# Performance work log

Hardware: AMD Instinct MI355X
Metric: run time of the kernel (lower is better)

The kernel has to match this reference:

```python
import jax, jax.numpy as jnp
import numpy as np

RHO = 0.5
MASK = 1.0
FR0 = 4096  # ifft length along fast-time axis
FR1 = 512   # fft length along slow-time (Doppler) axis
WIN = 8     # sliding-window length of the phase-reference accumulator
EPS_DENOM = 1e-6


def setup_inputs() -> dict:
    key = jax.random.key(0)
    k1, k2 = jax.random.split(key)
    x_real = jax.random.normal(k1, (8, 4096, 256), dtype=jnp.float32)
    x_imag = jax.random.normal(k2, (8, 4096, 256), dtype=jnp.float32)
    return {"x_real": x_real, "x_imag": x_imag}


def _phase_com_doppler(inp):
    # inp: [B, N, M_in] complex; ifft along last axis padded/truncated to FR0
    final = jnp.fft.ifft(inp, n=FR0, axis=2)  # [B, N, M]
    B, N, M = final.shape
    out0 = final[:, 0, :]                      # [B, M]
    # reproduces the torch `if k < 7` branch without control flow.
    buf0 = jnp.zeros((WIN, B, M), final.dtype).at[WIN - 1].set(out0)

    def step(carry, f_k1):
        pref, buf = carry
        s = jnp.sum(jnp.conj(pref) * f_k1, axis=-1, keepdims=True)  # [B,1]
        phase = s / jnp.abs(s)
        o = f_k1 * jnp.conj(phase)                                  # [B,M]
        pref = pref + o - buf[0]
        buf = jnp.concatenate([buf[1:], o[None]], axis=0)
        return (pref, buf), o

    seq = jnp.swapaxes(final, 0, 1)[1:]        # [N-1, B, M]
    _, outs = jax.lax.scan(step, (out0, buf0), seq)
    out = jnp.concatenate([out0[None], outs], axis=0)  # [N, B, M]
    out = jnp.swapaxes(out, 0, 1)              # [B, N, M]
    # fft along pulse axis padded to FR1
    return jnp.fft.fft(out, n=FR1, axis=1)     # [B, FR1, M]


def reference(x_real, x_imag):
    x = jax.lax.complex(x_real, x_imag)        # [B, P, Q] complex64
    denom = MASK + RHO
    denom = EPS_DENOM if denom == 0 else denom
    x2 = x * (1.0 / denom)
    out3 = _phase_com_doppler(jnp.swapaxes(x2, -1, -2))  # [B, FR1, FR0]
    out3 = jnp.swapaxes(out3, -1, -2)          # [B, FR0, FR1]
    # cs_data dict -> tuple ('input', 'nnline_input')
    return (x, out3)
```

## Files before the change

kernel.cpp:

```cpp
#include <hip/hip_runtime.h>
#include <math.h>

#define NF 4096
#define NC 256
#define NJ 512
#define CH 128
#define TWO_PI_F 6.28318530717958647692f

__device__ __forceinline__ float2 cmul(float2 a, float2 b) {
    return make_float2(a.x*b.x - a.y*b.y, a.x*b.y + a.y*b.x);
}

__device__ __forceinline__ void dft4i(float2& x0, float2& x1, float2& x2, float2& x3, float sgn) {
    float2 t0 = make_float2(x0.x + x2.x, x0.y + x2.y);
    float2 t1 = make_float2(x0.x - x2.x, x0.y - x2.y);
    float2 t2 = make_float2(x1.x + x3.x, x1.y + x3.y);
    float2 t3 = make_float2(x1.x - x3.x, x1.y - x3.y);
    float2 it3 = make_float2(-sgn * t3.y, sgn * t3.x);
    x0 = make_float2(t0.x + t2.x, t0.y + t2.y);
    x2 = make_float2(t0.x - t2.x, t0.y - t2.y);
    x1 = make_float2(t1.x + it3.x, t1.y + it3.y);
    x3 = make_float2(t1.x - it3.x, t1.y - it3.y);
}

__device__ __forceinline__ void dft16(float2* u, float sgn) {
    dft4i(u[0], u[4], u[8],  u[12], sgn);
    dft4i(u[1], u[5], u[9],  u[13], sgn);
    dft4i(u[2], u[6], u[10], u[14], sgn);
    dft4i(u[3], u[7], u[11], u[15], sgn);
    const float C1 = 0.9238795325112867f, S1 = 0.3826834323650898f, R2 = 0.7071067811865476f;
    u[5]  = cmul(u[5],  make_float2(C1,  sgn * S1));
    u[6]  = cmul(u[6],  make_float2(R2,  sgn * R2));
    u[7]  = cmul(u[7],  make_float2(S1,  sgn * C1));
    u[9]  = cmul(u[9],  make_float2(R2,  sgn * R2));
    u[10] = cmul(u[10], make_float2(0.f, sgn));
    u[11] = cmul(u[11], make_float2(-R2, sgn * R2));
    u[13] = cmul(u[13], make_float2(S1,  sgn * C1));
    u[14] = cmul(u[14], make_float2(-R2, sgn * R2));
    u[15] = cmul(u[15], make_float2(-C1, -sgn * S1));
    dft4i(u[0],  u[1],  u[2],  u[3],  sgn);
    dft4i(u[4],  u[5],  u[6],  u[7],  sgn);
    dft4i(u[8],  u[9],  u[10], u[11], sgn);
    dft4i(u[12], u[13], u[14], u[15], sgn);
}

__device__ __forceinline__ void dft8(const float2* u, float2* v, float sgn) {
    float2 e0 = u[0], e1 = u[2], e2 = u[4], e3 = u[6];
    float2 o0 = u[1], o1 = u[3], o2 = u[5], o3 = u[7];
    dft4i(e0, e1, e2, e3, sgn);
    dft4i(o0, o1, o2, o3, sgn);
    const float R2 = 0.7071067811865476f;
    float2 w1 = make_float2(R2, sgn * R2);
    float2 w2 = make_float2(0.f, sgn);
    float2 w3 = make_float2(-R2, sgn * R2);
    float2 t1 = cmul(o1, w1), t2 = cmul(o2, w2), t3 = cmul(o3, w3);
    v[0] = make_float2(e0.x + o0.x, e0.y + o0.y);
    v[4] = make_float2(e0.x - o0.x, e0.y - o0.y);
    v[1] = make_float2(e1.x + t1.x, e1.y + t1.y);
    v[5] = make_float2(e1.x - t1.x, e1.y - t1.y);
    v[2] = make_float2(e2.x + t2.x, e2.y + t2.y);
    v[6] = make_float2(e2.x - t2.x, e2.y - t2.y);
    v[3] = make_float2(e3.x + t3.x, e3.y + t3.y);
    v[7] = make_float2(e3.x - t3.x, e3.y - t3.y);
}

__global__ __launch_bounds__(256) void transpose_kernel(const float* __restrict__ xr,
                                                        const float* __restrict__ xi,
                                                        float2* __restrict__ fin,
                                                        int b0, int nbm1, int nbshift) {
    __shared__ float ldr[64][65];
    __shared__ float ldi[64][65];
    int wg = blockIdx.x;
    int bl = wg & nbm1;
    int rest = wg >> nbshift;
    int ft = rest & 63;
    int ct = rest >> 6;
    int f0 = ft << 6, c0 = ct << 6;
    int t = threadIdx.x;
    int cl = t & 63;
    int rq = t >> 6;
    const float scale = 1.0f / (4096.0f * 1.5f);
    int bg = b0 + bl;
    const float* xrb = xr + (size_t)bg * NF * NC;
    const float* xib = xi + (size_t)bg * NF * NC;
#pragma unroll
    for (int q = 0; q < 16; q++) {
        int r = q * 4 + rq;
        size_t idx = (size_t)(f0 + r) * NC + c0 + cl;
        ldr[cl][r] = xrb[idx] * scale;
        ldi[cl][r] = xib[idx] * scale;
    }
    __syncthreads();
    int fl = t & 63;
#pragma unroll
    for (int q = 0; q < 16; q++) {
        int cr = q * 4 + rq;
        fin[((size_t)(bl * NC + c0 + cr)) * NF + f0 + fl] =
            make_float2(ldr[cr][fl], ldi[cr][fl]);
    }
}

#define IPAD(a) ((a) + ((a) >> 4))

template<int P>
__device__ __forceinline__ void pass16(float2* S, int t, float sgn) {
    const int k = t & (P - 1);
    float2 u[16];
#pragma unroll
    for (int r = 0; r < 16; r++) u[r] = S[IPAD(t + 256 * r)];
    __syncthreads();
    if (P > 1) {
        float ab = sgn * (TWO_PI_F / (16.0f * (float)P)) * (float)k;
#pragma unroll
        for (int r = 1; r < 16; r++) {
            float sn, cs; __sincosf(ab * (float)r, &sn, &cs);
            u[r] = cmul(u[r], make_float2(cs, sn));
        }
    }
    dft16(u, sgn);
    const int base = 16 * P * (t / P) + k;
#pragma unroll
    for (int j = 0; j < 16; j++) {
        const int sl = ((j & 3) << 2) | (j >> 2);
        S[IPAD(base + j * P)] = u[sl];
    }
    __syncthreads();
}

__global__ __launch_bounds__(256) void ifft4096_kernel(float2* __restrict__ fin,
                                                       int bmask, int bshift) {
    __shared__ float2 S[4352];
    int wg = blockIdx.x;
    int bl = wg & bmask;
    int c = wg >> bshift;
    int t = threadIdx.x;
    size_t base = ((size_t)(bl * NC + c)) * NF;
#pragma unroll
    for (int q = 0; q < 16; q++) {
        int f = t + 256 * q;
        S[IPAD(f)] = fin[base + f];
    }
    __syncthreads();
    pass16<1>(S, t, 1.0f);
    pass16<16>(S, t, 1.0f);
    pass16<256>(S, t, 1.0f);
#pragma unroll
    for (int q = 0; q < 16; q++) {
        int f = t + 256 * q;
        fin[base + f] = S[IPAD(f)];
    }
}

__global__ __launch_bounds__(256) void gram_kernel(const float2* __restrict__ fin,
                                                   float2* __restrict__ gpart) {
    __shared__ float2 ring[16][CH];
    int wg = blockIdx.x;
    int bl = wg >> 7;
    int ch = (wg >> 2) & 31;
    int ks = wg & 3;
    int m0 = ch * CH;
    int k0 = ks * 64;
    int kend = k0 + 64;
    int t = threadIdx.x;
    int dgrp = t >> 5;
    int lane = t & 31;
    for (int r = (k0 >= 8 ? k0 - 8 : 0); r <= k0; r++)
        if (t < CH) ring[r & 15][t] = fin[((size_t)(bl * NC + r)) * NF + m0 + t];
    __syncthreads();
    for (int k = k0; k < kend; k++) {
        float2 nxt;
        bool ld = (k + 1 < kend) && (t < CH);
        if (ld) nxt = fin[((size_t)(bl * NC + k + 1)) * NF + m0 + t];
        int d = dgrp + 1;
        float2 acc = make_float2(0.f, 0.f);
        if (k - d >= 0) {
            int sk = k & 15, sj = (k - d) & 15;
#pragma unroll
            for (int i = 0; i < 4; i++) {
                int m = lane + 32 * i;
                float2 a = ring[sj][m];
                float2 bb = ring[sk][m];
                acc.x += a.x * bb.x + a.y * bb.y;
                acc.y += a.x * bb.y - a.y * bb.x;
            }
        }
#pragma unroll
        for (int off = 16; off >= 1; off >>= 1) {
            acc.x += __shfl_xor(acc.x, off);
            acc.y += __shfl_xor(acc.y, off);
        }
        if (lane == 0)
            gpart[((size_t)(bl * 32 + ch) * NC + k) * 8 + dgrp] = acc;
        if (ld) ring[(k + 1) & 15][t] = nxt;
        __syncthreads();
    }
}

__global__ void gsum_kernel(const float2* __restrict__ gpart, float2* __restrict__ gs, int total) {
    int e = blockIdx.x * blockDim.x + threadIdx.x;
    if (e >= total) return;
    int bl = e >> 11;
    int kd = e & 2047;
    float2 s = make_float2(0.f, 0.f);
    for (int ch = 0; ch < 32; ch++) {
        float2 v = gpart[((size_t)(bl * 32 + ch)) * 2048 + kd];
        s.x += v.x; s.y += v.y;
    }
    gs[e] = s;
}

#define SCAN_STEP(A0, A1, A2, A3, KIDX)  do {                                  \
    float rx0 = p1.x*A0.x - p1.y*A0.y, ry0 = p1.x*A0.y + p1.y*A0.x;            \
    float rx1 = p2.x*A0.z - p2.y*A0.w, ry1 = p2.x*A0.w + p2.y*A0.z;            \
    float rx2 = p3.x*A1.x - p3.y*A1.y, ry2 = p3.x*A1.y + p3.y*A1.x;            \
    float rx3 = p4.x*A1.z - p4.y*A1.w, ry3 = p4.x*A1.w + p4.y*A1.z;            \
    float rx4 = p5.x*A2.x - p5.y*A2.y, ry4 = p5.x*A2.y + p5.y*A2.x;            \
    float rx5 = p6.x*A2.z - p6.y*A2.w, ry5 = p6.x*A2.w + p6.y*A2.z;            \
    float rx6 = p7.x*A3.x - p7.y*A3.y, ry6 = p7.x*A3.y + p7.y*A3.x;            \
    float rx7 = p8.x*A3.z - p8.y*A3.w, ry7 = p8.x*A3.w + p8.y*A3.z;            \
    float sx = ((rx0 + rx1) + (rx2 + rx3)) + ((rx4 + rx5) + (rx6 + rx7));      \
    float sy = ((ry0 + ry1) + (ry2 + ry3)) + ((ry4 + ry5) + (ry6 + ry7));      \
    float inv = rsqrtf(sx * sx + sy * sy);                                     \
    float2 np = make_float2(sx * inv, sy * inv);                               \
    phase[t * NC + (KIDX)] = np;                                               \
    p8 = p7; p7 = p6; p6 = p5; p5 = p4; p4 = p3; p3 = p2; p2 = p1; p1 = np;    \
} while (0)

#define SCAN_LOADG4(BUF, KBASE)  do {                                          \
    _Pragma("unroll") for (int j = 0; j < 4; j++) {                            \
        _Pragma("unroll") for (int q = 0; q < 4; q++)                          \
            BUF[j][q] = gb4[((KBASE) + j) * 4 + q];                            \
    }                                                                          \
} while (0)

#define SCAN_GRP4(BUF, KBASE, FIRST)  do {                                     \
    _Pragma("unroll") for (int j = 0; j < 4; j++) {                            \
        if (FIRST && j == 0) {                                                 \
            phase[t * NC] = make_float2(1.f, 0.f);                             \
        } else {                                                               \
            SCAN_STEP(BUF[j][0], BUF[j][1], BUF[j][2], BUF[j][3], (KBASE) + j);\
        }                                                                      \
    }                                                                          \
} while (0)

__global__ __launch_bounds__(64, 1) void scan_copy_kernel(const float2* __restrict__ gs,
                                                          float2* __restrict__ phase, int nb,
                                                          const float4* __restrict__ csrc,
                                                          float4* __restrict__ cdst, int cn4) {
    if (blockIdx.x != 0) {
        int i = (blockIdx.x - 1) * 64 + threadIdx.x;
        int stride = (gridDim.x - 1) * 64;
        for (; i < cn4; i += stride) cdst[i] = csrc[i];
        return;
    }
    int t = threadIdx.x;
    if (t >= nb) return;
    const float4* gb4 = (const float4*)(gs + (size_t)t * 2048);
    float2 z = make_float2(0.f, 0.f);
    float2 p1 = make_float2(1.f, 0.f);
    float2 p2 = z, p3 = z, p4 = z, p5 = z, p6 = z, p7 = z, p8 = z;
    float4 GA[4][4], GB[4][4];
    SCAN_LOADG4(GA, 0);
    for (int g2 = 0; g2 < 32; g2++) {
        int k0 = g2 * 8;
        SCAN_LOADG4(GB, k0 + 4);
        __builtin_amdgcn_sched_barrier(0);
        if (g2 == 0) { SCAN_GRP4(GA, k0, true); } else { SCAN_GRP4(GA, k0, false); }
        if (g2 < 31) SCAN_LOADG4(GA, k0 + 8);
        __builtin_amdgcn_sched_barrier(0);
        SCAN_GRP4(GB, k0 + 4, false);
    }
}

__global__ void scale_kernel(float4* __restrict__ fin4, const float2* __restrict__ phase, int n4) {
    int i = blockIdx.x * blockDim.x + threadIdx.x;
    if (i >= n4) return;
    int row = i >> 11;
    float2 ph = phase[row];
    float4 v = fin4[i];
    fin4[i] = make_float4(v.x*ph.x + v.y*ph.y, v.y*ph.x - v.x*ph.y,
                          v.z*ph.x + v.w*ph.y, v.w*ph.x - v.z*ph.y);
}

#define FPAD 516

template<int P, bool ZTOP>
__device__ __forceinline__ void pass8x(float2* L, int fp, int i2, float sgn) {
    const int ia = i2, ib = i2 + 32;
    const int ka = ia & (P - 1), kb = ib & (P - 1);
    float2 ua[8], ub[8];
#pragma unroll
    for (int r = 0; r < 8; r++) {
        if (ZTOP && r >= 4) {
            ua[r] = make_float2(0.f, 0.f);
            ub[r] = make_float2(0.f, 0.f);
        } else {
            ua[r] = L[fp * FPAD + ia + 64 * r];
            ub[r] = L[fp * FPAD + ib + 64 * r];
        }
    }
    __syncthreads();
    if (P > 1) {
        float aba = sgn * (TWO_PI_F / (8.0f * (float)P)) * (float)ka;
        float abb = sgn * (TWO_PI_F / (8.0f * (float)P)) * (float)kb;
#pragma unroll
        for (int r = 1; r < 8; r++) {
            float sn, cs;
            __sincosf(aba * (float)r, &sn, &cs);
            ua[r] = cmul(ua[r], make_float2(cs, sn));
            __sincosf(abb * (float)r, &sn, &cs);
            ub[r] = cmul(ub[r], make_float2(cs, sn));
        }
    }
    float2 va[8], vb[8];
    dft8(ua, va, sgn);
    dft8(ub, vb, sgn);
    const int basea = 8 * P * (ia / P) + ka;
    const int baseb = 8 * P * (ib / P) + kb;
#pragma unroll
    for (int r = 0; r < 8; r++) {
        L[fp * FPAD + basea + r * P] = va[r];
        L[fp * FPAD + baseb + r * P] = vb[r];
    }
    __syncthreads();
}

__global__ __launch_bounds__(256) void fft512_kernel(const float2* __restrict__ fin,
                                                     const float2* __restrict__ ph,
                                                     float* __restrict__ outr,
                                                     float2* __restrict__ outc,
                                                     int b0, int realOnly) {
    __shared__ float2 L[8 * FPAD];
    int wg = blockIdx.x;
    int bl = wg >> 9;
    int f0 = (wg & 511) * 8;
    int t = threadIdx.x;
    int fpp = t & 7;
    int cg = t >> 3;
#pragma unroll
    for (int it = 0; it < 8; it++) {
        int c = it * 32 + cg;
        float2 v = fin[((size_t)(bl * NC + c)) * NF + f0 + fpp];
        if (ph) {
            float2 p = ph[bl * NC + c];
            v = make_float2(v.x * p.x + v.y * p.y, v.y * p.x - v.x * p.y);
        }
        L[fpp * FPAD + c] = v;
    }
    __syncthreads();
    int fp = t & 7;
    int i2 = t >> 3;
    pass8x<1, true >(L, fp, i2, -1.0f);
    pass8x<8, false>(L, fp, i2, -1.0f);
    pass8x<64, false>(L, fp, i2, -1.0f);
    size_t ob = ((size_t)((b0 + bl) * NF + f0)) * NJ;
    if (realOnly) {
#pragma unroll
        for (int fp2 = 0; fp2 < 8; fp2++)
#pragma unroll
            for (int jq = 0; jq < 2; jq++) {
                int j = t + 256 * jq;
                outr[ob + (size_t)fp2 * NJ + j] = L[fp2 * FPAD + j].x;
            }
    } else {
#pragma unroll
        for (int fp2 = 0; fp2 < 8; fp2++)
#pragma unroll
            for (int jq = 0; jq < 2; jq++) {
                int j = t + 256 * jq;
                outc[ob + (size_t)fp2 * NJ + j] = L[fp2 * FPAD + j];
            }
    }
}

__global__ void copy_kernel(const float4* __restrict__ src, float4* __restrict__ dst, int n4) {
    int i = blockIdx.x * blockDim.x + threadIdx.x;
    int stride = gridDim.x * blockDim.x;
    for (; i < n4; i += stride) dst[i] = src[i];
}
__global__ void pack_x_kernel(const float2* __restrict__ xr, const float2* __restrict__ xi,
                              float4* __restrict__ out, int n4) {
    int i = blockIdx.x * blockDim.x + threadIdx.x;
    int stride = gridDim.x * blockDim.x;
    for (; i < n4; i += stride) {
        float2 r = xr[i], m = xi[i];
        out[i] = make_float4(r.x, m.x, r.y, m.y);
    }
}

extern "C" void kernel_launch(void* const* d_in, const int* in_sizes, int n_in,
                              void* d_out, int out_size, void* d_ws, size_t ws_size,
                              hipStream_t stream) {
    const float* xr = (const float*)d_in[0];
    const float* xi = (const float*)d_in[1];
    float* out = (float*)d_out;

    if (out_size < 40000000) {
        float* out0r = out;
        float* out3r = out + 8388608;
        size_t need = (size_t)(8388608 + 524288 + 16384 + 2048) * sizeof(float2);
        if (ws_size >= need) {
            float2* fin   = (float2*)d_ws;
            float2* gpart = fin + 8388608;
            float2* gsb   = gpart + 524288;
            float2* phase = gsb + 16384;
            transpose_kernel<<<8 * 256, 256, 0, stream>>>(xr, xi, fin, 0, 7, 3);
            ifft4096_kernel<<<8 * NC, 256, 0, stream>>>(fin, 7, 3);
            gram_kernel<<<8 * 128, 256, 0, stream>>>(fin, gpart);
            gsum_kernel<<<(8 * 2048) / 256, 256, 0, stream>>>(gpart, gsb, 8 * 2048);
            scan_copy_kernel<<<2049, 64, 0, stream>>>(gsb, phase, 8,
                                                      (const float4*)xr, (float4*)out0r, 2097152);
            fft512_kernel<<<8 * 512, 256, 0, stream>>>(fin, phase, out3r, nullptr, 0, 1);
        } else {
            float2* fin   = (float2*)out0r;
            float2* o3f2  = (float2*)out3r;
            float2* gpart = o3f2 + (8388608 - 262144 - 8192 - 1024);
            float2* gsb   = o3f2 + (8388608 - 8192 - 1024);
            float2* phase = o3f2 + (8388608 - 1024);
            for (int p = 0; p < 2; p++) {
                int b0 = p * 4;
                transpose_kernel<<<4 * 256, 256, 0, stream>>>(xr, xi, fin, b0, 3, 2);
                ifft4096_kernel<<<4 * NC, 256, 0, stream>>>(fin, 3, 2);
                gram_kernel<<<4 * 128, 256, 0, stream>>>(fin, gpart);
                gsum_kernel<<<(4 * 2048) / 256, 256, 0, stream>>>(gpart, gsb, 4 * 2048);
                scan_copy_kernel<<<1, 64, 0, stream>>>(gsb, phase, 4, nullptr, nullptr, 0);
                scale_kernel<<<4 * 2048, 256, 0, stream>>>((float4*)fin, phase, 4 * 524288);
                fft512_kernel<<<4 * 512, 256, 0, stream>>>(fin, nullptr, out3r, nullptr, b0, 1);
            }
            copy_kernel<<<2048, 256, 0, stream>>>((const float4*)xr, (float4*)out0r, 2097152);
        }
    } else {
        float2* out0f2 = (float2*)out;
        float2* out3f2 = (float2*)(out + 16777216);
        float2* fin   = out0f2;
        float2* gpart = out3f2 + (16777216 - 524288 - 16384 - 2048);
        float2* gsb   = out3f2 + (16777216 - 16384 - 2048);
        float2* phase = out3f2 + (16777216 - 2048);
        transpose_kernel<<<8 * 256, 256, 0, stream>>>(xr, xi, fin, 0, 7, 3);
        ifft4096_kernel<<<8 * NC, 256, 0, stream>>>(fin, 7, 3);
        gram_kernel<<<8 * 128, 256, 0, stream>>>(fin, gpart);
        gsum_kernel<<<(8 * 2048) / 256, 256, 0, stream>>>(gpart, gsb, 8 * 2048);
        scan_copy_kernel<<<1, 64, 0, stream>>>(gsb, phase, 8, nullptr, nullptr, 0);
        scale_kernel<<<8 * 2048, 256, 0, stream>>>((float4*)fin, phase, 8 * 524288);
        fft512_kernel<<<8 * 512, 256, 0, stream>>>(fin, nullptr, nullptr, out3f2, 0, 0);
        pack_x_kernel<<<4096, 256, 0, stream>>>((const float2*)xr, (const float2*)xi,
                                                (float4*)out0f2, 4194304);
    }
}
```

Before: 188.4 us.

## Load gram tile into split real/imag LDS once, drop per-step barriers

```diff
diff --git a/kernel.cpp b/kernel.cpp
--- a/kernel.cpp
+++ b/kernel.cpp
@@ -151,37 +151,49 @@
     }
 }
 
+#define GSTR 129
 __global__ __launch_bounds__(256) void gram_kernel(const float2* __restrict__ fin,
                                                    float2* __restrict__ gpart) {
-    __shared__ float2 ring[16][CH];
+    __shared__ float lre[40 * GSTR];
+    __shared__ float lim[40 * GSTR];
     int wg = blockIdx.x;
-    int bl = wg >> 7;
-    int ch = (wg >> 2) & 31;
-    int ks = wg & 3;
+    int bl = wg >> 8;
+    int ks = (wg >> 5) & 7;
+    int ch = wg & 31;
     int m0 = ch * CH;
-    int k0 = ks * 64;
-    int kend = k0 + 64;
+    int k0 = ks * 32;
     int t = threadIdx.x;
+#pragma unroll
+    for (int q = 0; q < 20; q++) {
+        int e = t + 256 * q;
+        int row = e >> 7;
+        int m = e & 127;
+        int gk = k0 - 8 + row;
+        float2 v = (gk >= 0) ? fin[((size_t)(bl * NC + gk)) * NF + m0 + m]
+                             : make_float2(0.f, 0.f);
+        lre[row * GSTR + m] = v.x;
+        lim[row * GSTR + m] = v.y;
+    }
+    __syncthreads();
     int dgrp = t >> 5;
     int lane = t & 31;
-    for (int r = (k0 >= 8 ? k0 - 8 : 0); r <= k0; r++)
-        if (t < CH) ring[r & 15][t] = fin[((size_t)(bl * NC + r)) * NF + m0 + t];
-    __syncthreads();
-    for (int k = k0; k < kend; k++) {
-        float2 nxt;
-        bool ld = (k + 1 < kend) && (t < CH);
-        if (ld) nxt = fin[((size_t)(bl * NC + k + 1)) * NF + m0 + t];
-        int d = dgrp + 1;
+    int d = dgrp + 1;
+#pragma unroll
+    for (int kk = 0; kk < 32; kk++) {
+        int k = k0 + kk;
         float2 acc = make_float2(0.f, 0.f);
         if (k - d >= 0) {
-            int sk = k & 15, sj = (k - d) & 15;
+            const float* ar = &lre[(kk + 8 - d) * GSTR];
+            const float* ai = &lim[(kk + 8 - d) * GSTR];
+            const float* br = &lre[(kk + 8) * GSTR];
+            const float* bi = &lim[(kk + 8) * GSTR];
 #pragma unroll
             for (int i = 0; i < 4; i++) {
                 int m = lane + 32 * i;
-                float2 a = ring[sj][m];
-                float2 bb = ring[sk][m];
-                acc.x += a.x * bb.x + a.y * bb.y;
-                acc.y += a.x * bb.y - a.y * bb.x;
+                float ax = ar[m], ay = ai[m];
+                float bx = br[m], by = bi[m];
+                acc.x += ax * bx + ay * by;
+                acc.y += ax * by - ay * bx;
             }
         }
 #pragma unroll
@@ -191,8 +203,6 @@
         }
         if (lane == 0)
             gpart[((size_t)(bl * 32 + ch) * NC + k) * 8 + dgrp] = acc;
-        if (ld) ring[(k + 1) & 15][t] = nxt;
-        __syncthreads();
     }
 }
 
@@ -406,7 +416,7 @@
             float2* phase = gsb + 16384;
             transpose_kernel<<<8 * 256, 256, 0, stream>>>(xr, xi, fin, 0, 7, 3);
             ifft4096_kernel<<<8 * NC, 256, 0, stream>>>(fin, 7, 3);
-            gram_kernel<<<8 * 128, 256, 0, stream>>>(fin, gpart);
+            gram_kernel<<<8 * 256, 256, 0, stream>>>(fin, gpart);
             gsum_kernel<<<(8 * 2048) / 256, 256, 0, stream>>>(gpart, gsb, 8 * 2048);
             scan_copy_kernel<<<2049, 64, 0, stream>>>(gsb, phase, 8,
                                                       (const float4*)xr, (float4*)out0r, 2097152);
@@ -421,7 +431,7 @@
                 int b0 = p * 4;
                 transpose_kernel<<<4 * 256, 256, 0, stream>>>(xr, xi, fin, b0, 3, 2);
                 ifft4096_kernel<<<4 * NC, 256, 0, stream>>>(fin, 3, 2);
-                gram_kernel<<<4 * 128, 256, 0, stream>>>(fin, gpart);
+                gram_kernel<<<4 * 256, 256, 0, stream>>>(fin, gpart);
                 gsum_kernel<<<(4 * 2048) / 256, 256, 0, stream>>>(gpart, gsb, 4 * 2048);
                 scan_copy_kernel<<<1, 64, 0, stream>>>(gsb, phase, 4, nullptr, nullptr, 0);
                 scale_kernel<<<4 * 2048, 256, 0, stream>>>((float4*)fin, phase, 4 * 524288);
@@ -438,7 +448,7 @@
         float2* phase = out3f2 + (16777216 - 2048);
         transpose_kernel<<<8 * 256, 256, 0, stream>>>(xr, xi, fin, 0, 7, 3);
         ifft4096_kernel<<<8 * NC, 256, 0, stream>>>(fin, 7, 3);
-        gram_kernel<<<8 * 128, 256, 0, stream>>>(fin, gpart);
+        gram_kernel<<<8 * 256, 256, 0, stream>>>(fin, gpart);
         gsum_kernel<<<(8 * 2048) / 256, 256, 0, stream>>>(gpart, gsb, 8 * 2048);
         scan_copy_kernel<<<1, 64, 0, stream>>>(gsb, phase, 8, nullptr, nullptr, 0);
         scale_kernel<<<8 * 2048, 256, 0, stream>>>((float4*)fin, phase, 8 * 524288);
```

After: 186.7 us. Within noise of the previous version (-0.9%).
